# Performance work log

Hardware: AMD Instinct MI355X
Metric: run time of the kernel (lower is better)

Reference implementation:

```python
import jax, jax.numpy as jnp
import numpy as np

D_MAIN = 256
D_HID = 512  # int(d_main * d_multiplier)
N_NUM = 96
B = 1024
N_CAND = 100000
LN_EPS = 1e-5


def _ln(x, g, b):
    mu = x.mean(-1, keepdims=True)
    var = ((x - mu) ** 2).mean(-1, keepdims=True)
    return (x - mu) / jnp.sqrt(var + LN_EPS) * g + b


def _block(x, W1, b1, W2, b2):
    # Linear -> ReLU -> (Dropout=id) -> Linear -> (Dropout=id), residual added by caller
    return jnp.maximum(x @ W1 + b1, 0.0) @ W2 + b2


def setup_inputs() -> dict:
    key = jax.random.key(0)
    ks = jax.random.split(key, 32)

    def w(i, shape):
        fan_in = shape[0]
        return jax.random.normal(ks[i], shape, jnp.float32) / np.sqrt(fan_in)

    return {
        "x_num": jax.random.normal(ks[0], (B, N_NUM), jnp.float32),
        "cand_x_num": jax.random.normal(ks[1], (N_CAND, N_NUM), jnp.float32),
        "cand_y": jax.random.normal(ks[2], (N_CAND, 1), jnp.float32),
        "context_size": 96,
        # input linear
        "W_in": w(3, (N_NUM, D_MAIN)), "b_in": jnp.zeros((D_MAIN,), jnp.float32),
        # encoder block (no norm: first block)
        "We1": w(4, (D_MAIN, D_HID)), "be1": jnp.zeros((D_HID,), jnp.float32),
        "We2": w(5, (D_HID, D_MAIN)), "be2": jnp.zeros((D_MAIN,), jnp.float32),
        # mixer LayerNorm (mixer_normalization='auto' with encoder_n_blocks>0)
        "g_m": jnp.ones((D_MAIN,), jnp.float32), "b_m": jnp.zeros((D_MAIN,), jnp.float32),
        # S: key projection
        "Ws": w(6, (D_MAIN, D_MAIN)), "bs": jnp.zeros((D_MAIN,), jnp.float32),
        "Wy": w(7, (1, D_MAIN)), "by": jnp.zeros((D_MAIN,), jnp.float32),
        # V_t: Linear(no bias) -> ReLU -> Linear
        "Wt1": w(8, (D_MAIN, D_HID)),
        "Wt2": w(9, (D_HID, D_MAIN)), "bt2": jnp.zeros((D_MAIN,), jnp.float32),
        # predictor block (no norm: first block)
        "Wp1": w(10, (D_MAIN, D_HID)), "bp1": jnp.zeros((D_HID,), jnp.float32),
        "Wp2": w(11, (D_HID, D_MAIN)), "bp2": jnp.zeros((D_MAIN,), jnp.float32),
        # head P: LayerNorm -> ReLU -> Linear(d_main, 1)
        "g_h": jnp.ones((D_MAIN,), jnp.float32), "b_h": jnp.zeros((D_MAIN,), jnp.float32),
        "Wh": w(12, (D_MAIN, 1)), "bh": jnp.zeros((1,), jnp.float32),
    }


def _encode(x, W_in, b_in, We1, be1, We2, be2, g_m, b_m, Ws, bs):
    h = x @ W_in + b_in
    h = h + _block(h, We1, be1, We2, be2)
    k = _ln(h, g_m, b_m) @ Ws + bs
    return h, k


def reference(x_num, cand_x_num, cand_y, context_size,
              W_in, b_in, We1, be1, We2, be2, g_m, b_m, Ws, bs,
              Wy, by, Wt1, Wt2, bt2, Wp1, bp1, Wp2, bp2, g_h, b_h, Wh, bh):
    # encode queries and candidates with shared weights
    x, k = _encode(x_num, W_in, b_in, We1, be1, We2, be2, g_m, b_m, Ws, bs)
    _, ck = _encode(cand_x_num, W_in, b_in, We1, be1, We2, be2, g_m, b_m, Ws, bs)

    # similarities = -||k - ck||^2  [B, N_CAND]
    sim = (2.0 * (k @ ck.T)
           - (k * k).sum(-1, keepdims=True)
           - (ck * ck).sum(-1)[None, :])

    top_sim, idx = jax.lax.top_k(sim, context_size)   # [B, m]
    probs = jax.nn.softmax(top_sim, axis=-1)           # context_dropout = id in eval

    ctx_k = ck[idx]                                    # [B, m, d_main]
    ctx_y = cand_y[idx]                                # [B, m, 1]

    # values = V_y(y) + V_t(k - ctx_k)
    v = (ctx_y @ Wy + by
         + jnp.maximum((k[:, None, :] - ctx_k) @ Wt1, 0.0) @ Wt2 + bt2)

    x = x + jnp.einsum('bm,bmd->bd', probs, v)

    # predictor block + head
    x = x + _block(x, Wp1, bp1, Wp2, bp2)
    out = jnp.maximum(_ln(x, g_h, b_h), 0.0) @ Wh + bh  # [B, 1]
    return out
```

## Files before the change

### kernel.cpp

```cpp
#include <hip/hip_runtime.h>
#include <stdint.h>

#define NCAND 100000
#define NB    1024
#define DNUM  96
#define DM    256
#define DH    512
#define MCTX  96
#define LNEPS 1e-5f

typedef __bf16 bf16x8 __attribute__((ext_vector_type(8)));
typedef float  f32x4  __attribute__((ext_vector_type(4)));
typedef unsigned short u16x8 __attribute__((ext_vector_type(8)));
typedef unsigned short us;

__device__ __forceinline__ us f2bf(float x)
{
    unsigned u = __float_as_uint(x);
    unsigned r = u + 0x7FFFu + ((u >> 16) & 1u);
    return (us)(r >> 16);
}
__device__ __forceinline__ float bfbits(us h)
{
    return __uint_as_float(((unsigned)h) << 16);
}

extern "C" __global__ __launch_bounds__(256)
void split_k(const float* X, us* Xh, us* Xl, long long n)
{
    long long i = (long long)blockIdx.x * 256 + threadIdx.x;
    if (i < n) {
        float x = X[i];
        us h = f2bf(x);
        Xh[i] = h;
        Xl[i] = f2bf(x - bfbits(h));
    }
}

extern "C" __global__ __launch_bounds__(256)
void packW_k(const float* W, us* Ph, us* Pl, int Kd, int Nd)
{
    int i = blockIdx.x * 256 + threadIdx.x;
    if (i >= Kd * Nd) return;
    int e = i & 7, lane = (i >> 3) & 63, r = i >> 9;
    int KT = Kd >> 5;
    int kt = r % KT, jt = r / KT;
    int n = jt * 16 + (lane & 15);
    int k = kt * 32 + (lane >> 4) * 8 + e;
    float x = W[(long long)k * Nd + n];
    us h = f2bf(x);
    Ph[i] = h;
    Pl[i] = f2bf(x - bfbits(h));
}

extern "C" __global__ __launch_bounds__(256)
void packR_k(const us* Rh, const us* Rl, us* Ph, us* Pl, int Kd, int total)
{
    int i = blockIdx.x * 256 + threadIdx.x;
    if (i >= total) return;
    int e = i & 7, lane = (i >> 3) & 63, r = i >> 9;
    int KT = Kd >> 5;
    int kt = r % KT, jt = r / KT;
    int n = jt * 16 + (lane & 15);
    int k = kt * 32 + (lane >> 4) * 8 + e;
    Ph[i] = Rh[(long long)n * Kd + k];
    Pl[i] = Rl[(long long)n * Kd + k];
}

extern "C" __global__ __launch_bounds__(256)
void gemm_d(const us* Ah, const us* Al, const us* BPh, const us* BPl,
            float* outF, us* outH, us* outL, us* outB16,
            const float* bias, const us* Rh, const us* Rl, int dorelu,
            const float* lng, const float* lnb, us* lnH, us* lnL,
            float* snOut,
            const us* Gqh, const us* Gql, const us* Gch, const us* Gcl,
            const int* gidx,
            float* simT, const float* colb,
            int M, int N, int K)
{
    int t = threadIdx.x, wave = t >> 6, lane = t & 63;
    int lm = lane & 15, lk = (lane >> 4) * 8, rb = (lane >> 4) * 4;
    int m0 = blockIdx.x * 64 + wave * 16;
    int n0 = blockIdx.y * 256;
    int arow = m0 + lm;
    int KT = K >> 5;

    f32x4 acc[16];
#pragma unroll
    for (int j = 0; j < 16; j++)
        for (int e = 0; e < 4; e++) acc[j][e] = 0.0f;

    int gb = 0, gc = 0;
    if (gidx && arow < M) { gb = arow / MCTX; gc = gidx[arow]; }

    for (int kt = 0; kt < KT; kt++) {
        int k0 = kt * 32;
        u16x8 au = {0,0,0,0,0,0,0,0}, alu = au;
        if (arow < M) {
            if (!gidx) {
                au  = *(const u16x8*)(Ah + (long long)arow * K + k0 + lk);
                alu = *(const u16x8*)(Al + (long long)arow * K + k0 + lk);
            } else {
                u16x8 qh = *(const u16x8*)(Gqh + (long long)gb * DM + k0 + lk);
                u16x8 ql = *(const u16x8*)(Gql + (long long)gb * DM + k0 + lk);
                u16x8 ch = *(const u16x8*)(Gch + (long long)gc * DM + k0 + lk);
                u16x8 cl = *(const u16x8*)(Gcl + (long long)gc * DM + k0 + lk);
#pragma unroll
                for (int e = 0; e < 8; e++) {
                    float v = (bfbits(qh[e]) + bfbits(ql[e]))
                            - (bfbits(ch[e]) + bfbits(cl[e]));
                    au[e] = f2bf(v);
                }
            }
        }
        bf16x8 fah = *(bf16x8*)&au;
        bf16x8 fal = *(bf16x8*)&alu;
#pragma unroll
        for (int j = 0; j < 16; j++) {
            long long bo = ((long long)((n0 >> 4) + j) * KT + kt) * 512 + lane * 8;
            u16x8 bu  = *(const u16x8*)(BPh + bo);
            u16x8 blu = *(const u16x8*)(BPl + bo);
            bf16x8 fbh = *(bf16x8*)&bu;
            bf16x8 fbl = *(bf16x8*)&blu;
            acc[j] = __builtin_amdgcn_mfma_f32_16x16x32_bf16(fah, fbh, acc[j], 0, 0, 0);
            acc[j] = __builtin_amdgcn_mfma_f32_16x16x32_bf16(fah, fbl, acc[j], 0, 0, 0);
            if (!gidx)
                acc[j] = __builtin_amdgcn_mfma_f32_16x16x32_bf16(fal, fbh, acc[j], 0, 0, 0);
        }
    }

    if (simT) {
        if (m0 < M) {
#pragma unroll
            for (int j = 0; j < 16; j++) {
                int q = n0 + j * 16 + lm;
                f32x4 v;
                for (int e = 0; e < 4; e++)
                    v[e] = 2.0f * acc[j][e] - colb[m0 + rb + e];
                *(f32x4*)(simT + (long long)q * NCAND + m0 + rb) = v;
            }
        }
        return;
    }

#pragma unroll
    for (int j = 0; j < 16; j++) {
        int col = n0 + j * 16 + lm;
        float bc = bias ? bias[col] : 0.0f;
        for (int e = 0; e < 4; e++) {
            int row = m0 + rb + e;
            float v = acc[j][e] + bc;
            if (row < M) {
                long long oix = (long long)row * N + col;
                if (Rh) v += bfbits(Rh[oix]) + bfbits(Rl[oix]);
                if (dorelu && v < 0.0f) v = 0.0f;
                if (outF)   outF[oix] = v;
                if (outB16) outB16[oix] = f2bf(v);
                if (outH) { us h = f2bf(v); outH[oix] = h; outL[oix] = f2bf(v - bfbits(h)); }
            } else {
                if (dorelu && v < 0.0f) v = 0.0f;
            }
            acc[j][e] = v;
        }
    }

    if (lng || snOut) {
        float mu4[4], rs4[4];
        for (int e = 0; e < 4; e++) {
            float s1 = 0.0f, s2 = 0.0f;
#pragma unroll
            for (int j = 0; j < 16; j++) { float v = acc[j][e]; s1 += v; s2 += v * v; }
            for (int o = 1; o < 16; o <<= 1) {
                s1 += __shfl_xor(s1, o, 64);
                s2 += __shfl_xor(s2, o, 64);
            }
            int row = m0 + rb + e;
            if (snOut && lm == 0 && row < M) snOut[row] = s2;
            float mu = s1 * (1.0f / 256.0f);
            float var = s2 * (1.0f / 256.0f) - mu * mu;
            mu4[e] = mu;
            rs4[e] = rsqrtf(var + LNEPS);
        }
        if (lng) {
#pragma unroll
            for (int j = 0; j < 16; j++) {
                int col = n0 + j * 16 + lm;
                float g = lng[col], bb = lnb[col];
                for (int e = 0; e < 4; e++) {
                    int row = m0 + rb + e;
                    if (row >= M) continue;
                    float y = (acc[j][e] - mu4[e]) * rs4[e] * g + bb;
                    long long oix = (long long)row * N + col;
                    us h = f2bf(y);
                    lnH[oix] = h;
                    lnL[oix] = f2bf(y - bfbits(h));
                }
            }
        }
    }
}

__device__ unsigned fmapf(float f)
{
    unsigned u = __float_as_uint(f);
    return u ^ (unsigned)(((int)u >> 31) | (int)0x80000000);
}

extern "C" __global__ __launch_bounds__(1024)
void topk_k(const float* S, int q0, int* out_idx, float* out_p)
{
    int t = threadIdx.x;
    const float* row = S + (long long)blockIdx.x * NCAND;
    const float4* row4 = (const float4*)row;
    __shared__ int hist8[8][256];
    __shared__ unsigned sh_prefix;
    __shared__ int sh_want, cntG, cntE;
    __shared__ int   gidx[128];
    __shared__ float gval[128];
    __shared__ int   eqi[2048];
    __shared__ float vals[MCTX];
    __shared__ int   inds[MCTX];
    __shared__ float pr[MCTX];

    if (t == 0) { sh_prefix = 0u; sh_want = MCTX; cntG = 0; cntE = 0; }

    for (int lvl = 0; lvl < 4; lvl++) {
        int shift = 24 - 8 * lvl;
        for (int i = t; i < 2048; i += 1024) ((int*)hist8)[i] = 0;
        __syncthreads();
        unsigned prefix = sh_prefix;
        unsigned mask = (lvl == 0) ? 0u : (0xFFFFFFFFu << (shift + 8));
        int* hrow = hist8[t & 7];
        for (int c = t; c < NCAND / 4; c += 1024) {
            float4 v = row4[c];
            unsigned k0 = fmapf(v.x), k1 = fmapf(v.y), k2 = fmapf(v.z), k3 = fmapf(v.w);
            if ((k0 & mask) == prefix) atomicAdd(&hrow[(k0 >> shift) & 255], 1);
            if ((k1 & mask) == prefix) atomicAdd(&hrow[(k1 >> shift) & 255], 1);
            if ((k2 & mask) == prefix) atomicAdd(&hrow[(k2 >> shift) & 255], 1);
            if ((k3 & mask) == prefix) atomicAdd(&hrow[(k3 >> shift) & 255], 1);
        }
        __syncthreads();
        if (t < 256) {
            int s = 0;
            for (int g2 = 1; g2 < 8; g2++) s += hist8[g2][t];
            hist8[0][t] += s;
        }
        __syncthreads();
        if (t == 0) {
            int want = sh_want, cum = 0;
            for (int b2 = 255; b2 >= 0; b2--) {
                cum += hist8[0][b2];
                if (cum >= want) {
                    sh_want = want - (cum - hist8[0][b2]);
                    sh_prefix = prefix | ((unsigned)b2 << shift);
                    break;
                }
            }
        }
        __syncthreads();
    }
    unsigned T = sh_prefix;
    for (int c = t; c < NCAND / 4; c += 1024) {
        float4 v = row4[c];
        float vv[4]; vv[0] = v.x; vv[1] = v.y; vv[2] = v.z; vv[3] = v.w;
        for (int e = 0; e < 4; e++) {
            unsigned key = fmapf(vv[e]);
            if (key > T) {
                int p = atomicAdd(&cntG, 1);
                if (p < 128) { gidx[p] = c * 4 + e; gval[p] = vv[e]; }
            } else if (key == T) {
                int p = atomicAdd(&cntE, 1);
                if (p < 2048) eqi[p] = c * 4 + e;
            }
        }
    }
    __syncthreads();
    if (t == 0) {
        int nG = cntG; if (nG > MCTX) nG = MCTX;
        int nE = cntE; if (nE > 2048) nE = 2048;
        int need = MCTX - nG;
        for (int i = 0; i < nG; i++) { inds[i] = gidx[i]; vals[i] = gval[i]; }
        for (int s = 0; s < need; s++) {
            int best = 0x7FFFFFFF, bp = -1;
            for (int e = 0; e < nE; e++) if (eqi[e] < best) { best = eqi[e]; bp = e; }
            if (bp >= 0) { eqi[bp] = 0x7FFFFFFF; inds[nG + s] = best; vals[nG + s] = row[best]; }
            else         { inds[nG + s] = 0;     vals[nG + s] = -3.0e38f; }
        }
        float mx = -3.4e38f;
        for (int i = 0; i < MCTX; i++) if (vals[i] > mx) mx = vals[i];
        float sum = 0.0f;
        for (int i = 0; i < MCTX; i++) { float e = expf(vals[i] - mx); pr[i] = e; sum += e; }
        float inv = 1.0f / sum;
        for (int i = 0; i < MCTX; i++) pr[i] *= inv;
    }
    __syncthreads();
    if (t < MCTX) {
        long long o = (long long)(q0 + blockIdx.x) * MCTX + t;
        out_idx[o] = inds[t];
        out_p[o]   = pr[t];
    }
}

extern "C" __global__ __launch_bounds__(256)
void ybar_k(const float* P, const int* idx, const float* y, float* ybar)
{
    __shared__ float sred[256];
    int b = blockIdx.x, t = threadIdx.x;
    float v = 0.0f;
    if (t < MCTX) v = P[(long long)b * MCTX + t] * y[idx[(long long)b * MCTX + t]];
    sred[t] = v; __syncthreads();
    for (int s = 128; s > 0; s >>= 1) { if (t < s) sred[t] += sred[t + s]; __syncthreads(); }
    if (t == 0) ybar[b] = sred[0];
}

extern "C" __global__ __launch_bounds__(512)
void wsum2_k(const float* Pq, const float* R, const float* P, const int* idx, float* u)
{
    __shared__ float pl[MCTX];
    __shared__ int ix[MCTX];
    int b = blockIdx.x, j = threadIdx.x;
    if (j < MCTX) {
        pl[j] = P[(long long)b * MCTX + j];
        ix[j] = idx[(long long)b * MCTX + j];
    }
    __syncthreads();
    float pb = Pq[(long long)b * DH + j];
    float a = 0.0f;
    for (int m = 0; m < MCTX; m++) {
        float d = pb - R[(long long)ix[m] * DH + j];
        a += pl[m] * (d > 0.0f ? d : 0.0f);
    }
    u[(long long)b * DH + j] = a;
}

extern "C" __global__ __launch_bounds__(512)
void wsum_k(const us* U, const float* P, float* u)
{
    __shared__ float pl[MCTX];
    int b = blockIdx.x, j = threadIdx.x;
    if (j < MCTX) pl[j] = P[(long long)b * MCTX + j];
    __syncthreads();
    const us* Ub = U + (long long)b * MCTX * DH;
    float acc = 0.0f;
    for (int m = 0; m < MCTX; m++) acc += pl[m] * bfbits(Ub[(long long)m * DH + j]);
    u[(long long)b * DH + j] = acc;
}

extern "C" __global__ __launch_bounds__(256)
void mixprep_sp(us* h2h, us* h2l, const float* ybar,
                const float* Wy, const float* by, const float* bt2)
{
    int b = blockIdx.x, d = threadIdx.x;
    long long i = (long long)b * DM + d;
    float v = bfbits(h2h[i]) + bfbits(h2l[i]) + ybar[b] * Wy[d] + by[d] + bt2[d];
    us h = f2bf(v);
    h2h[i] = h;
    h2l[i] = f2bf(v - bfbits(h));
}

extern "C" __global__ __launch_bounds__(256)
void head_k(const float* X, const float* g, const float* bln, const float* Wh,
            const float* bh, float* out)
{
    __shared__ float sred[256];
    int r = blockIdx.x, t = threadIdx.x;
    float x = X[(long long)r * DM + t];
    sred[t] = x; __syncthreads();
    for (int s = 128; s > 0; s >>= 1) { if (t < s) sred[t] += sred[t + s]; __syncthreads(); }
    float mu = sred[0] * (1.0f / DM); __syncthreads();
    float d = x - mu;
    sred[t] = d * d; __syncthreads();
    for (int s = 128; s > 0; s >>= 1) { if (t < s) sred[t] += sred[t + s]; __syncthreads(); }
    float var = sred[0] * (1.0f / DM); __syncthreads();
    float ln = d * rsqrtf(var + LNEPS) * g[t] + bln[t];
    float rl = (ln > 0.0f) ? ln : 0.0f;
    sred[t] = rl * Wh[t]; __syncthreads();
    for (int s = 128; s > 0; s >>= 1) { if (t < s) sred[t] += sred[t + s]; __syncthreads(); }
    if (t == 0) out[r] = sred[0] + bh[0];
}

#define ZU (us*)0
#define ZCU (const us*)0
#define ZF (float*)0
#define ZCF (const float*)0
#define ZI (const int*)0

extern "C" void kernel_launch(void* const* d_in, const int* in_sizes, int n_in,
                              void* d_out, int out_size, void* d_ws, size_t ws_size,
                              hipStream_t stream)
{
    const float* x_num  = (const float*)d_in[0];
    const float* cand_x = (const float*)d_in[1];
    const float* cand_y = (const float*)d_in[2];
    const float* W_in = (const float*)d_in[4];
    const float* b_in = (const float*)d_in[5];
    const float* We1  = (const float*)d_in[6];
    const float* be1  = (const float*)d_in[7];
    const float* We2  = (const float*)d_in[8];
    const float* be2  = (const float*)d_in[9];
    const float* g_m  = (const float*)d_in[10];
    const float* b_m  = (const float*)d_in[11];
    const float* Ws   = (const float*)d_in[12];
    const float* bs   = (const float*)d_in[13];
    const float* Wy   = (const float*)d_in[14];
    const float* by   = (const float*)d_in[15];
    const float* Wt1  = (const float*)d_in[16];
    const float* Wt2  = (const float*)d_in[17];
    const float* bt2  = (const float*)d_in[18];
    const float* Wp1  = (const float*)d_in[19];
    const float* bp1  = (const float*)d_in[20];
    const float* Wp2  = (const float*)d_in[21];
    const float* bp2  = (const float*)d_in[22];
    const float* g_h  = (const float*)d_in[23];
    const float* b_h  = (const float*)d_in[24];
    const float* Wh   = (const float*)d_in[25];
    const float* bh   = (const float*)d_in[26];
    float* out = (float*)d_out;

    char* p = (char*)d_ws;
    us* WinPh = (us*)p; p += 256*96*2;   us* WinPl = (us*)p; p += 256*96*2;
    us* We1Ph = (us*)p; p += 512*256*2;  us* We1Pl = (us*)p; p += 512*256*2;
    us* We2Ph = (us*)p; p += 256*512*2;  us* We2Pl = (us*)p; p += 256*512*2;
    us* WsPh  = (us*)p; p += 256*256*2;  us* WsPl  = (us*)p; p += 256*256*2;
    us* Wt1Ph = (us*)p; p += 512*256*2;  us* Wt1Pl = (us*)p; p += 512*256*2;
    us* Wt2Ph = (us*)p; p += 256*512*2;  us* Wt2Pl = (us*)p; p += 256*512*2;
    us* Wp1Ph = (us*)p; p += 512*256*2;  us* Wp1Pl = (us*)p; p += 512*256*2;
    us* Wp2Ph = (us*)p; p += 256*512*2;  us* Wp2Pl = (us*)p; p += 256*512*2;
    us* XNh  = (us*)p; p += (long long)NB*DNUM*2;  us* XNl  = (us*)p; p += (long long)NB*DNUM*2;
    us* HQ1h = (us*)p; p += (long long)NB*DM*2;    us* HQ1l = (us*)p; p += (long long)NB*DM*2;
    us* TQh  = (us*)p; p += (long long)NB*DH*2;    us* TQl  = (us*)p; p += (long long)NB*DH*2;
    us* HQ2h = (us*)p; p += (long long)NB*DM*2;    us* HQ2l = (us*)p; p += (long long)NB*DM*2;
    us* LNQh = (us*)p; p += (long long)NB*DM*2;    us* LNQl = (us*)p; p += (long long)NB*DM*2;
    us* KQh  = (us*)p; p += (long long)NB*DM*2;    us* KQl  = (us*)p; p += (long long)NB*DM*2;
    us* KQPh = (us*)p; p += (long long)NB*DM*2;    us* KQPl = (us*)p; p += (long long)NB*DM*2;
    us* XQh  = (us*)p; p += (long long)NB*DM*2;    us* XQl  = (us*)p; p += (long long)NB*DM*2;
    us* UQvh = (us*)p; p += (long long)NB*DH*2;    us* UQvl = (us*)p; p += (long long)NB*DH*2;
    float* UQv  = (float*)p; p += (long long)NB*DH*4;
    float* Pq   = (float*)p; p += (long long)NB*DH*4;
    float* XQ2f = (float*)p; p += (long long)NB*DM*4;
    float* YB   = (float*)p; p += (long long)NB*4;
    int*   IDX  = (int*)p;   p += (long long)NB*MCTX*4;
    float* PRB  = (float*)p; p += (long long)NB*MCTX*4;
    us* KCh = (us*)p; p += (long long)NCAND*DM*2;  us* KCl = (us*)p; p += (long long)NCAND*DM*2;
    float* SC = (float*)p; p += (long long)NCAND*4;

    size_t used = (size_t)(p - (char*)d_ws);
    long long avail = (ws_size > used + 4096) ? (long long)(ws_size - used - 4096) : 0;
    int EC = 6250;
    if      (avail >= 243300000LL) EC = 50000;
    else if (avail >= 141000000LL) EC = 25000;
    else if (avail >=  89700000LL) EC = 12500;
    int QS = (avail >= 204800000LL) ? 512 : 256;
    int tierA = (avail >= 204800000LL) ? 1 : 0;
    int VC = (avail >= 100700000LL) ? 1024 : 512;

    char* AR = p;
    us* CXh = (us*)AR;
    us* CXl = CXh + (long long)NCAND*DNUM;
    char* EB = AR + (long long)NCAND*DNUM*4;
    us* Hch  = (us*)EB;                              us* Hcl  = Hch + (long long)EC*DM;
    us* Tch  = (us*)(EB + (long long)EC*DM*4);       us* Tcl  = Tch + (long long)EC*DH;
    us* LNch = (us*)(EB + (long long)EC*(DM+DH)*4);  us* LNcl = LNch + (long long)EC*DM;
    float* Sb = (float*)AR;
    float* R  = (float*)AR;
    us* Ub = (us*)AR;

    dim3 blk(256);

    packW_k<<<dim3((DNUM*DM+255)/256), blk, 0, stream>>>(W_in, WinPh, WinPl, DNUM, DM);
    packW_k<<<dim3((DM*DH+255)/256), blk, 0, stream>>>(We1, We1Ph, We1Pl, DM, DH);
    packW_k<<<dim3((DH*DM+255)/256), blk, 0, stream>>>(We2, We2Ph, We2Pl, DH, DM);
    packW_k<<<dim3((DM*DM+255)/256), blk, 0, stream>>>(Ws,  WsPh,  WsPl,  DM, DM);
    packW_k<<<dim3((DM*DH+255)/256), blk, 0, stream>>>(Wt1, Wt1Ph, Wt1Pl, DM, DH);
    packW_k<<<dim3((DH*DM+255)/256), blk, 0, stream>>>(Wt2, Wt2Ph, Wt2Pl, DH, DM);
    packW_k<<<dim3((DM*DH+255)/256), blk, 0, stream>>>(Wp1, Wp1Ph, Wp1Pl, DM, DH);
    packW_k<<<dim3((DH*DM+255)/256), blk, 0, stream>>>(Wp2, Wp2Ph, Wp2Pl, DH, DM);
    split_k<<<dim3((NB*DNUM+255)/256), blk, 0, stream>>>(x_num, XNh, XNl, (long long)NB*DNUM);
    split_k<<<dim3((NCAND*DNUM+255)/256), blk, 0, stream>>>(cand_x, CXh, CXl, (long long)NCAND*DNUM);

    gemm_d<<<dim3(NB/64, 1), blk, 0, stream>>>(XNh, XNl, WinPh, WinPl,
        ZF, HQ1h, HQ1l, ZU, b_in, ZCU, ZCU, 0, ZCF, ZCF, ZU, ZU, ZF,
        ZCU, ZCU, ZCU, ZCU, ZI, ZF, ZCF, NB, DM, DNUM);
    gemm_d<<<dim3(NB/64, 2), blk, 0, stream>>>(HQ1h, HQ1l, We1Ph, We1Pl,
        ZF, TQh, TQl, ZU, be1, ZCU, ZCU, 1, ZCF, ZCF, ZU, ZU, ZF,
        ZCU, ZCU, ZCU, ZCU, ZI, ZF, ZCF, NB, DH, DM);
    gemm_d<<<dim3(NB/64, 1), blk, 0, stream>>>(TQh, TQl, We2Ph, We2Pl,
        ZF, HQ2h, HQ2l, ZU, be2, HQ1h, HQ1l, 0, g_m, b_m, LNQh, LNQl, ZF,
        ZCU, ZCU, ZCU, ZCU, ZI, ZF, ZCF, NB, DM, DH);
    gemm_d<<<dim3(NB/64, 1), blk, 0, stream>>>(LNQh, LNQl, WsPh, WsPl,
        ZF, KQh, KQl, ZU, bs, ZCU, ZCU, 0, ZCF, ZCF, ZU, ZU, ZF,
        ZCU, ZCU, ZCU, ZCU, ZI, ZF, ZCF, NB, DM, DM);
    packR_k<<<dim3((NB*DM+255)/256), blk, 0, stream>>>(KQh, KQl, KQPh, KQPl, DM, NB*DM);

    for (int c0 = 0; c0 < NCAND; c0 += EC) {
        int gx = (EC + 63) / 64;
        gemm_d<<<dim3(gx, 1), blk, 0, stream>>>(CXh + (long long)c0*DNUM, CXl + (long long)c0*DNUM,
            WinPh, WinPl, ZF, Hch, Hcl, ZU, b_in, ZCU, ZCU, 0, ZCF, ZCF, ZU, ZU, ZF,
            ZCU, ZCU, ZCU, ZCU, ZI, ZF, ZCF, EC, DM, DNUM);
        gemm_d<<<dim3(gx, 2), blk, 0, stream>>>(Hch, Hcl, We1Ph, We1Pl,
            ZF, Tch, Tcl, ZU, be1, ZCU, ZCU, 1, ZCF, ZCF, ZU, ZU, ZF,
            ZCU, ZCU, ZCU, ZCU, ZI, ZF, ZCF, EC, DH, DM);
        gemm_d<<<dim3(gx, 1), blk, 0, stream>>>(Tch, Tcl, We2Ph, We2Pl,
            ZF, ZU, ZU, ZU, be2, Hch, Hcl, 0, g_m, b_m, LNch, LNcl, ZF,
            ZCU, ZCU, ZCU, ZCU, ZI, ZF, ZCF, EC, DM, DH);
        gemm_d<<<dim3(gx, 1), blk, 0, stream>>>(LNch, LNcl, WsPh, WsPl,
            ZF, KCh + (long long)c0*DM, KCl + (long long)c0*DM, ZU, bs, ZCU, ZCU, 0,
            ZCF, ZCF, ZU, ZU, SC + c0,
            ZCU, ZCU, ZCU, ZCU, ZI, ZF, ZCF, EC, DM, DM);
    }

    for (int q0 = 0; q0 < NB; q0 += QS) {
        gemm_d<<<dim3((NCAND + 63) / 64, QS / 256), blk, 0, stream>>>(KCh, KCl,
            KQPh + (long long)q0*DM, KQPl + (long long)q0*DM,
            ZF, ZU, ZU, ZU, ZCF, ZCU, ZCU, 0, ZCF, ZCF, ZU, ZU, ZF,
            ZCU, ZCU, ZCU, ZCU, ZI, Sb, SC, NCAND, QS, DM);
        topk_k<<<dim3(QS), dim3(1024), 0, stream>>>(Sb, q0, IDX, PRB);
    }

    ybar_k<<<dim3(NB), blk, 0, stream>>>(PRB, IDX, cand_y, YB);
    gemm_d<<<dim3(NB/64, 2), blk, 0, stream>>>(KQh, KQl, Wt1Ph, Wt1Pl,
        Pq, ZU, ZU, ZU, ZCF, ZCU, ZCU, 0, ZCF, ZCF, ZU, ZU, ZF,
        ZCU, ZCU, ZCU, ZCU, ZI, ZF, ZCF, NB, DH, DM);
    if (tierA) {
        gemm_d<<<dim3((NCAND + 63) / 64, 2), blk, 0, stream>>>(KCh, KCl, Wt1Ph, Wt1Pl,
            R, ZU, ZU, ZU, ZCF, ZCU, ZCU, 0, ZCF, ZCF, ZU, ZU, ZF,
            ZCU, ZCU, ZCU, ZCU, ZI, ZF, ZCF, NCAND, DH, DM);
        wsum2_k<<<dim3(NB), dim3(512), 0, stream>>>(Pq, R, PRB, IDX, UQv);
    } else {
        for (int v0 = 0; v0 < NB; v0 += VC) {
            gemm_d<<<dim3((VC * MCTX) / 64, 2), blk, 0, stream>>>(ZCU, ZCU, Wt1Ph, Wt1Pl,
                ZF, ZU, ZU, Ub, ZCF, ZCU, ZCU, 1, ZCF, ZCF, ZU, ZU, ZF,
                KQh + (long long)v0*DM, KQl + (long long)v0*DM, KCh, KCl,
                IDX + (long long)v0*MCTX, ZF, ZCF, VC * MCTX, DH, DM);
            wsum_k<<<dim3(VC), dim3(512), 0, stream>>>(Ub, PRB + (long long)v0*MCTX,
                                                       UQv + (long long)v0*DH);
        }
    }
    split_k<<<dim3((NB*DH+255)/256), blk, 0, stream>>>(UQv, UQvh, UQvl, (long long)NB*DH);
    mixprep_sp<<<dim3(NB), blk, 0, stream>>>(HQ2h, HQ2l, YB, Wy, by, bt2);
    gemm_d<<<dim3(NB/64, 1), blk, 0, stream>>>(UQvh, UQvl, Wt2Ph, Wt2Pl,
        ZF, XQh, XQl, ZU, ZCF, HQ2h, HQ2l, 0, ZCF, ZCF, ZU, ZU, ZF,
        ZCU, ZCU, ZCU, ZCU, ZI, ZF, ZCF, NB, DM, DH);

    gemm_d<<<dim3(NB/64, 2), blk, 0, stream>>>(XQh, XQl, Wp1Ph, Wp1Pl,
        ZF, TQh, TQl, ZU, bp1, ZCU, ZCU, 1, ZCF, ZCF, ZU, ZU, ZF,
        ZCU, ZCU, ZCU, ZCU, ZI, ZF, ZCF, NB, DH, DM);
    gemm_d<<<dim3(NB/64, 1), blk, 0, stream>>>(TQh, TQl, Wp2Ph, Wp2Pl,
        XQ2f, ZU, ZU, ZU, bp2, XQh, XQl, 0, ZCF, ZCF, ZU, ZU, ZF,
        ZCU, ZCU, ZCU, ZCU, ZI, ZF, ZCF, NB, DM, DH);
    head_k<<<dim3(NB), blk, 0, stream>>>(XQ2f, g_h, b_h, Wh, bh, out);
}
```

Before: 3.561 ms.

## Use 12-bit radix pass with compacted candidate refinement in top-k; stage A tiles in LDS

The top-k kernel replaces four full passes of 8-bit radix histograms over the 100k similarity row with one 12-bit histogram pass. Elements in the boundary bin are compacted into shared memory, and the remaining radix levels run only on that small set, with a fallback to full-row passes when the set overflows. The aim is to cut repeated global reads and atomics per row. Separately, the GEMM now loads the A tile cooperatively into LDS and reads fragments from there, which adds two barriers per k-step.

```diff
diff --git a/kernel.cpp b/kernel.cpp
--- a/kernel.cpp
+++ b/kernel.cpp
@@ -8,6 +8,7 @@
 #define DH    512
 #define MCTX  96
 #define LNEPS 1e-5f
+#define ECAP  2560
 
 typedef __bf16 bf16x8 __attribute__((ext_vector_type(8)));
 typedef float  f32x4  __attribute__((ext_vector_type(4)));
@@ -78,11 +79,13 @@
             float* simT, const float* colb,
             int M, int N, int K)
 {
+    __shared__ us Ahs[64][40];
+    __shared__ us Als[64][40];
     int t = threadIdx.x, wave = t >> 6, lane = t & 63;
     int lm = lane & 15, lk = (lane >> 4) * 8, rb = (lane >> 4) * 4;
-    int m0 = blockIdx.x * 64 + wave * 16;
+    int m0b = blockIdx.x * 64;
+    int m0 = m0b + wave * 16;
     int n0 = blockIdx.y * 256;
-    int arow = m0 + lm;
     int KT = K >> 5;
 
     f32x4 acc[16];
@@ -90,31 +93,38 @@
     for (int j = 0; j < 16; j++)
         for (int e = 0; e < 4; e++) acc[j][e] = 0.0f;
 
+    int sr = t >> 2;
+    int ss = (t & 3) * 8;
+    int srow = m0b + sr;
     int gb = 0, gc = 0;
-    if (gidx && arow < M) { gb = arow / MCTX; gc = gidx[arow]; }
+    if (gidx && srow < M) { gb = srow / MCTX; gc = gidx[srow]; }
 
     for (int kt = 0; kt < KT; kt++) {
         int k0 = kt * 32;
-        u16x8 au = {0,0,0,0,0,0,0,0}, alu = au;
-        if (arow < M) {
+        u16x8 ah8 = {0,0,0,0,0,0,0,0}, al8 = ah8;
+        if (srow < M) {
             if (!gidx) {
-                au  = *(const u16x8*)(Ah + (long long)arow * K + k0 + lk);
-                alu = *(const u16x8*)(Al + (long long)arow * K + k0 + lk);
+                ah8 = *(const u16x8*)(Ah + (long long)srow * K + k0 + ss);
+                al8 = *(const u16x8*)(Al + (long long)srow * K + k0 + ss);
             } else {
-                u16x8 qh = *(const u16x8*)(Gqh + (long long)gb * DM + k0 + lk);
-                u16x8 ql = *(const u16x8*)(Gql + (long long)gb * DM + k0 + lk);
-                u16x8 ch = *(const u16x8*)(Gch + (long long)gc * DM + k0 + lk);
-                u16x8 cl = *(const u16x8*)(Gcl + (long long)gc * DM + k0 + lk);
+                u16x8 qh = *(const u16x8*)(Gqh + (long long)gb * DM + k0 + ss);
+                u16x8 ql = *(const u16x8*)(Gql + (long long)gb * DM + k0 + ss);
+                u16x8 ch = *(const u16x8*)(Gch + (long long)gc * DM + k0 + ss);
+                u16x8 cl = *(const u16x8*)(Gcl + (long long)gc * DM + k0 + ss);
 #pragma unroll
                 for (int e = 0; e < 8; e++) {
                     float v = (bfbits(qh[e]) + bfbits(ql[e]))
                             - (bfbits(ch[e]) + bfbits(cl[e]));
-                    au[e] = f2bf(v);
+                    ah8[e] = f2bf(v);
                 }
             }
         }
-        bf16x8 fah = *(bf16x8*)&au;
-        bf16x8 fal = *(bf16x8*)&alu;
+        __syncthreads();
+        *(u16x8*)&Ahs[sr][ss] = ah8;
+        *(u16x8*)&Als[sr][ss] = al8;
+        __syncthreads();
+        bf16x8 fah = *(const bf16x8*)&Ahs[wave * 16 + lm][lk];
+        bf16x8 fal = *(const bf16x8*)&Als[wave * 16 + lm][lk];
 #pragma unroll
         for (int j = 0; j < 16; j++) {
             long long bo = ((long long)((n0 >> 4) + j) * KT + kt) * 512 + lane * 8;
@@ -205,6 +215,11 @@
     unsigned u = __float_as_uint(f);
     return u ^ (unsigned)(((int)u >> 31) | (int)0x80000000);
 }
+__device__ float funmap(unsigned key)
+{
+    unsigned uu = (key & 0x80000000u) ? (key ^ 0x80000000u) : ~key;
+    return __uint_as_float(uu);
+}
 
 extern "C" __global__ __launch_bounds__(1024)
 void topk_k(const float* S, int q0, int* out_idx, float* out_p)
@@ -212,91 +227,165 @@
     int t = threadIdx.x;
     const float* row = S + (long long)blockIdx.x * NCAND;
     const float4* row4 = (const float4*)row;
-    __shared__ int hist8[8][256];
-    __shared__ unsigned sh_prefix;
-    __shared__ int sh_want, cntG, cntE;
-    __shared__ int   gidx[128];
-    __shared__ float gval[128];
-    __shared__ int   eqi[2048];
-    __shared__ float vals[MCTX];
-    __shared__ int   inds[MCTX];
+    __shared__ int hist[4096];
+    __shared__ unsigned ek0[ECAP]; __shared__ int ei0[ECAP];
+    __shared__ unsigned ek1[ECAP]; __shared__ int ei1[ECAP];
+    __shared__ float gv[MCTX]; __shared__ int gi[MCTX];
     __shared__ float pr[MCTX];
-
-    if (t == 0) { sh_prefix = 0u; sh_want = MCTX; cntG = 0; cntE = 0; }
-
-    for (int lvl = 0; lvl < 4; lvl++) {
-        int shift = 24 - 8 * lvl;
-        for (int i = t; i < 2048; i += 1024) ((int*)hist8)[i] = 0;
-        __syncthreads();
-        unsigned prefix = sh_prefix;
-        unsigned mask = (lvl == 0) ? 0u : (0xFFFFFFFFu << (shift + 8));
-        int* hrow = hist8[t & 7];
-        for (int c = t; c < NCAND / 4; c += 1024) {
-            float4 v = row4[c];
-            unsigned k0 = fmapf(v.x), k1 = fmapf(v.y), k2 = fmapf(v.z), k3 = fmapf(v.w);
-            if ((k0 & mask) == prefix) atomicAdd(&hrow[(k0 >> shift) & 255], 1);
-            if ((k1 & mask) == prefix) atomicAdd(&hrow[(k1 >> shift) & 255], 1);
-            if ((k2 & mask) == prefix) atomicAdd(&hrow[(k2 >> shift) & 255], 1);
-            if ((k3 & mask) == prefix) atomicAdd(&hrow[(k3 >> shift) & 255], 1);
-        }
-        __syncthreads();
-        if (t < 256) {
-            int s = 0;
-            for (int g2 = 1; g2 < 8; g2++) s += hist8[g2][t];
-            hist8[0][t] += s;
-        }
-        __syncthreads();
-        if (t == 0) {
-            int want = sh_want, cum = 0;
-            for (int b2 = 255; b2 >= 0; b2--) {
-                cum += hist8[0][b2];
-                if (cum >= want) {
-                    sh_want = want - (cum - hist8[0][b2]);
-                    sh_prefix = prefix | ((unsigned)b2 << shift);
-                    break;
-                }
-            }
-        }
-        __syncthreads();
-    }
-    unsigned T = sh_prefix;
+    __shared__ int gcnt, ecnt, encnt, sh_b, sh_need;
+
+    if (t == 0) { gcnt = 0; ecnt = 0; }
+    for (int i = t; i < 4096; i += 1024) hist[i] = 0;
+    __syncthreads();
+
+    for (int c = t; c < NCAND / 4; c += 1024) {
+        float4 v = row4[c];
+        atomicAdd(&hist[fmapf(v.x) >> 20], 1);
+        atomicAdd(&hist[fmapf(v.y) >> 20], 1);
+        atomicAdd(&hist[fmapf(v.z) >> 20], 1);
+        atomicAdd(&hist[fmapf(v.w) >> 20], 1);
+    }
+    __syncthreads();
+    if (t == 0) {
+        int cum = 0, b = 4095;
+        for (; b >= 0; b--) { cum += hist[b]; if (cum >= MCTX) break; }
+        sh_b = b; sh_need = MCTX - (cum - hist[b]);
+    }
+    __syncthreads();
+    unsigned b1 = (unsigned)sh_b;
     for (int c = t; c < NCAND / 4; c += 1024) {
         float4 v = row4[c];
         float vv[4]; vv[0] = v.x; vv[1] = v.y; vv[2] = v.z; vv[3] = v.w;
         for (int e = 0; e < 4; e++) {
             unsigned key = fmapf(vv[e]);
-            if (key > T) {
-                int p = atomicAdd(&cntG, 1);
-                if (p < 128) { gidx[p] = c * 4 + e; gval[p] = vv[e]; }
-            } else if (key == T) {
-                int p = atomicAdd(&cntE, 1);
-                if (p < 2048) eqi[p] = c * 4 + e;
+            unsigned bin = key >> 20;
+            if (bin > b1) {
+                int p = atomicAdd(&gcnt, 1);
+                gv[p] = vv[e]; gi[p] = c * 4 + e;
+            } else if (bin == b1) {
+                int p = atomicAdd(&ecnt, 1);
+                if (p < ECAP) { ek0[p] = key; ei0[p] = c * 4 + e; }
             }
         }
     }
     __syncthreads();
+    unsigned pref = b1 << 20;
+    int shifts[3]; shifts[0] = 12; shifts[1] = 4; shifts[2] = 0;
+    int widths[3]; widths[0] = 256; widths[1] = 256; widths[2] = 16;
+
+    if (ecnt <= ECAP) {
+        int n = ecnt;
+        unsigned* ksrc = ek0; int* isrc = ei0;
+        unsigned* kdst = ek1; int* idst = ei1;
+        for (int lvl = 0; lvl < 3; lvl++) {
+            int sh = shifts[lvl], nb = widths[lvl];
+            unsigned msk = (unsigned)(nb - 1);
+            for (int i = t; i < nb; i += 1024) hist[i] = 0;
+            if (t == 0) encnt = 0;
+            __syncthreads();
+            for (int i = t; i < n; i += 1024)
+                atomicAdd(&hist[(ksrc[i] >> sh) & msk], 1);
+            __syncthreads();
+            if (t == 0) {
+                int need = sh_need, cum = 0, b = nb - 1;
+                for (; b >= 0; b--) { cum += hist[b]; if (cum >= need) break; }
+                sh_b = b; sh_need = need - (cum - hist[b]);
+            }
+            __syncthreads();
+            unsigned bl = (unsigned)sh_b;
+            for (int i = t; i < n; i += 1024) {
+                unsigned bin = (ksrc[i] >> sh) & msk;
+                if (bin > bl) {
+                    int p = atomicAdd(&gcnt, 1);
+                    gv[p] = funmap(ksrc[i]); gi[p] = isrc[i];
+                } else if (bin == bl) {
+                    int p = atomicAdd(&encnt, 1);
+                    kdst[p] = ksrc[i]; idst[p] = isrc[i];
+                }
+            }
+            __syncthreads();
+            pref |= bl << sh;
+            n = encnt;
+            unsigned* tk = ksrc; ksrc = kdst; kdst = tk;
+            int* ti = isrc; isrc = idst; idst = ti;
+            __syncthreads();
+        }
+        if (t == 0) {
+            int need = sh_need;
+            float tv = funmap(pref);
+            for (int s = 0; s < need; s++) {
+                int best = 0x7FFFFFFF, bp = -1;
+                for (int i2 = 0; i2 < n; i2++) if (isrc[i2] < best) { best = isrc[i2]; bp = i2; }
+                int p = gcnt + s;
+                if (bp >= 0) { isrc[bp] = 0x7FFFFFFF; gv[p] = tv; gi[p] = best; }
+                else         { gv[p] = -3.0e38f; gi[p] = 0; }
+            }
+        }
+        __syncthreads();
+    } else {
+        unsigned mask = 0xFFF00000u;
+        for (int lvl = 0; lvl < 3; lvl++) {
+            int sh = shifts[lvl], nb = widths[lvl];
+            unsigned msk = (unsigned)(nb - 1);
+            for (int i = t; i < nb; i += 1024) hist[i] = 0;
+            __syncthreads();
+            for (int c = t; c < NCAND; c += 1024) {
+                unsigned key = fmapf(row[c]);
+                if ((key & mask) == pref) atomicAdd(&hist[(key >> sh) & msk], 1);
+            }
+            __syncthreads();
+            if (t == 0) {
+                int need = sh_need, cum = 0, b = nb - 1;
+                for (; b >= 0; b--) { cum += hist[b]; if (cum >= need) break; }
+                sh_b = b; sh_need = need - (cum - hist[b]);
+            }
+            __syncthreads();
+            pref |= ((unsigned)sh_b) << sh;
+            mask |= msk << sh;
+            __syncthreads();
+        }
+        if (t == 0) encnt = 0;
+        __syncthreads();
+        for (int c = t; c < NCAND; c += 1024) {
+            unsigned key = fmapf(row[c]);
+            if ((key >> 20) == b1) {
+                if (key > pref) {
+                    int p = atomicAdd(&gcnt, 1);
+                    gv[p] = row[c]; gi[p] = c;
+                } else if (key == pref) {
+                    int p = atomicAdd(&encnt, 1);
+                    if (p < ECAP) ei1[p] = c;
+                }
+            }
+        }
+        __syncthreads();
+        if (t == 0) {
+            int need = sh_need;
+            int n = encnt; if (n > ECAP) n = ECAP;
+            float tv = funmap(pref);
+            for (int s = 0; s < need; s++) {
+                int best = 0x7FFFFFFF, bp = -1;
+                for (int i2 = 0; i2 < n; i2++) if (ei1[i2] < best) { best = ei1[i2]; bp = i2; }
+                int p = gcnt + s;
+                if (bp >= 0) { ei1[bp] = 0x7FFFFFFF; gv[p] = tv; gi[p] = best; }
+                else         { gv[p] = -3.0e38f; gi[p] = 0; }
+            }
+        }
+        __syncthreads();
+    }
+
     if (t == 0) {
-        int nG = cntG; if (nG > MCTX) nG = MCTX;
-        int nE = cntE; if (nE > 2048) nE = 2048;
-        int need = MCTX - nG;
-        for (int i = 0; i < nG; i++) { inds[i] = gidx[i]; vals[i] = gval[i]; }
-        for (int s = 0; s < need; s++) {
-            int best = 0x7FFFFFFF, bp = -1;
-            for (int e = 0; e < nE; e++) if (eqi[e] < best) { best = eqi[e]; bp = e; }
-            if (bp >= 0) { eqi[bp] = 0x7FFFFFFF; inds[nG + s] = best; vals[nG + s] = row[best]; }
-            else         { inds[nG + s] = 0;     vals[nG + s] = -3.0e38f; }
-        }
         float mx = -3.4e38f;
-        for (int i = 0; i < MCTX; i++) if (vals[i] > mx) mx = vals[i];
+        for (int i = 0; i < MCTX; i++) if (gv[i] > mx) mx = gv[i];
         float sum = 0.0f;
-        for (int i = 0; i < MCTX; i++) { float e = expf(vals[i] - mx); pr[i] = e; sum += e; }
+        for (int i = 0; i < MCTX; i++) { float e = expf(gv[i] - mx); pr[i] = e; sum += e; }
         float inv = 1.0f / sum;
         for (int i = 0; i < MCTX; i++) pr[i] *= inv;
     }
     __syncthreads();
     if (t < MCTX) {
         long long o = (long long)(q0 + blockIdx.x) * MCTX + t;
-        out_idx[o] = inds[t];
+        out_idx[o] = gi[t];
         out_p[o]   = pr[t];
     }
 }
```

Measured after the change: 3.946 ms. 1.11x slower.

## Retile GEMM waves to 64x64 subtiles for A/B fragment reuse

Applied to the files above, without the earlier changes.

Each wave now computes a 64-row by 64-column subtile (4x4 MFMA tiles) instead of 16 rows by 256 columns, so every loaded A fragment is reused across 4 B tiles and every B fragment across 4 A rows. This cuts per-wave B-fragment global loads from 16 to 4 per k-step, at the cost of 4 A-fragment loads (including the gathered difference computation). Row LayerNorm statistics now span waves, so a shared-memory cross-wave reduction with two barriers is added. The simT epilogue indexing changes accordingly.

```diff
diff --git a/kernel.cpp b/kernel.cpp
--- a/kernel.cpp
+++ b/kernel.cpp
@@ -78,122 +78,164 @@
             float* simT, const float* colb,
             int M, int N, int K)
 {
+    __shared__ float red1[256];
+    __shared__ float red2[256];
+    __shared__ float mu_s[64];
+    __shared__ float rs_s[64];
     int t = threadIdx.x, wave = t >> 6, lane = t & 63;
     int lm = lane & 15, lk = (lane >> 4) * 8, rb = (lane >> 4) * 4;
-    int m0 = blockIdx.x * 64 + wave * 16;
+    int m0b = blockIdx.x * 64;
     int n0 = blockIdx.y * 256;
-    int arow = m0 + lm;
     int KT = K >> 5;
-
-    f32x4 acc[16];
-#pragma unroll
-    for (int j = 0; j < 16; j++)
-        for (int e = 0; e < 4; e++) acc[j][e] = 0.0f;
-
-    int gb = 0, gc = 0;
-    if (gidx && arow < M) { gb = arow / MCTX; gc = gidx[arow]; }
+    int jt0 = (n0 >> 4) + wave * 4;
+
+    f32x4 acc[4][4];
+#pragma unroll
+    for (int i = 0; i < 4; i++)
+#pragma unroll
+        for (int j = 0; j < 4; j++)
+            for (int e = 0; e < 4; e++) acc[i][j][e] = 0.0f;
+
+    int gb4[4], gc4[4];
+    if (gidx) {
+#pragma unroll
+        for (int i = 0; i < 4; i++) {
+            int grow = m0b + i * 16 + lm;
+            if (grow < M) { gb4[i] = grow / MCTX; gc4[i] = gidx[grow]; }
+            else          { gb4[i] = 0; gc4[i] = 0; }
+        }
+    }
 
     for (int kt = 0; kt < KT; kt++) {
         int k0 = kt * 32;
-        u16x8 au = {0,0,0,0,0,0,0,0}, alu = au;
-        if (arow < M) {
-            if (!gidx) {
-                au  = *(const u16x8*)(Ah + (long long)arow * K + k0 + lk);
-                alu = *(const u16x8*)(Al + (long long)arow * K + k0 + lk);
-            } else {
-                u16x8 qh = *(const u16x8*)(Gqh + (long long)gb * DM + k0 + lk);
-                u16x8 ql = *(const u16x8*)(Gql + (long long)gb * DM + k0 + lk);
-                u16x8 ch = *(const u16x8*)(Gch + (long long)gc * DM + k0 + lk);
-                u16x8 cl = *(const u16x8*)(Gcl + (long long)gc * DM + k0 + lk);
-#pragma unroll
-                for (int e = 0; e < 8; e++) {
-                    float v = (bfbits(qh[e]) + bfbits(ql[e]))
-                            - (bfbits(ch[e]) + bfbits(cl[e]));
-                    au[e] = f2bf(v);
+        bf16x8 fah[4], fal[4];
+#pragma unroll
+        for (int i = 0; i < 4; i++) {
+            int arow = m0b + i * 16 + lm;
+            u16x8 ah8 = {0,0,0,0,0,0,0,0}, al8 = ah8;
+            if (arow < M) {
+                if (!gidx) {
+                    ah8 = *(const u16x8*)(Ah + (long long)arow * K + k0 + lk);
+                    al8 = *(const u16x8*)(Al + (long long)arow * K + k0 + lk);
+                } else {
+                    u16x8 qh = *(const u16x8*)(Gqh + (long long)gb4[i] * DM + k0 + lk);
+                    u16x8 ql = *(const u16x8*)(Gql + (long long)gb4[i] * DM + k0 + lk);
+                    u16x8 ch = *(const u16x8*)(Gch + (long long)gc4[i] * DM + k0 + lk);
+                    u16x8 cl = *(const u16x8*)(Gcl + (long long)gc4[i] * DM + k0 + lk);
+#pragma unroll
+                    for (int e = 0; e < 8; e++) {
+                        float v = (bfbits(qh[e]) + bfbits(ql[e]))
+                                - (bfbits(ch[e]) + bfbits(cl[e]));
+                        ah8[e] = f2bf(v);
+                    }
                 }
             }
-        }
-        bf16x8 fah = *(bf16x8*)&au;
-        bf16x8 fal = *(bf16x8*)&alu;
-#pragma unroll
-        for (int j = 0; j < 16; j++) {
-            long long bo = ((long long)((n0 >> 4) + j) * KT + kt) * 512 + lane * 8;
+            fah[i] = *(bf16x8*)&ah8;
+            fal[i] = *(bf16x8*)&al8;
+        }
+#pragma unroll
+        for (int j = 0; j < 4; j++) {
+            long long bo = ((long long)(jt0 + j) * KT + kt) * 512 + lane * 8;
             u16x8 bu  = *(const u16x8*)(BPh + bo);
             u16x8 blu = *(const u16x8*)(BPl + bo);
             bf16x8 fbh = *(bf16x8*)&bu;
             bf16x8 fbl = *(bf16x8*)&blu;
-            acc[j] = __builtin_amdgcn_mfma_f32_16x16x32_bf16(fah, fbh, acc[j], 0, 0, 0);
-            acc[j] = __builtin_amdgcn_mfma_f32_16x16x32_bf16(fah, fbl, acc[j], 0, 0, 0);
-            if (!gidx)
-                acc[j] = __builtin_amdgcn_mfma_f32_16x16x32_bf16(fal, fbh, acc[j], 0, 0, 0);
+#pragma unroll
+            for (int i = 0; i < 4; i++) {
+                acc[i][j] = __builtin_amdgcn_mfma_f32_16x16x32_bf16(fah[i], fbh, acc[i][j], 0, 0, 0);
+                acc[i][j] = __builtin_amdgcn_mfma_f32_16x16x32_bf16(fah[i], fbl, acc[i][j], 0, 0, 0);
+                if (!gidx)
+                    acc[i][j] = __builtin_amdgcn_mfma_f32_16x16x32_bf16(fal[i], fbh, acc[i][j], 0, 0, 0);
+            }
         }
     }
 
     if (simT) {
-        if (m0 < M) {
-#pragma unroll
-            for (int j = 0; j < 16; j++) {
-                int q = n0 + j * 16 + lm;
+#pragma unroll
+        for (int i = 0; i < 4; i++) {
+            int cb = m0b + i * 16;
+            if (cb >= M) break;
+#pragma unroll
+            for (int j = 0; j < 4; j++) {
+                int q = n0 + wave * 64 + j * 16 + lm;
                 f32x4 v;
                 for (int e = 0; e < 4; e++)
-                    v[e] = 2.0f * acc[j][e] - colb[m0 + rb + e];
-                *(f32x4*)(simT + (long long)q * NCAND + m0 + rb) = v;
+                    v[e] = 2.0f * acc[i][j][e] - colb[cb + rb + e];
+                *(f32x4*)(simT + (long long)q * NCAND + cb + rb) = v;
             }
         }
         return;
     }
 
 #pragma unroll
-    for (int j = 0; j < 16; j++) {
-        int col = n0 + j * 16 + lm;
+    for (int j = 0; j < 4; j++) {
+        int col = n0 + wave * 64 + j * 16 + lm;
         float bc = bias ? bias[col] : 0.0f;
-        for (int e = 0; e < 4; e++) {
-            int row = m0 + rb + e;
-            float v = acc[j][e] + bc;
-            if (row < M) {
-                long long oix = (long long)row * N + col;
-                if (Rh) v += bfbits(Rh[oix]) + bfbits(Rl[oix]);
-                if (dorelu && v < 0.0f) v = 0.0f;
-                if (outF)   outF[oix] = v;
-                if (outB16) outB16[oix] = f2bf(v);
-                if (outH) { us h = f2bf(v); outH[oix] = h; outL[oix] = f2bf(v - bfbits(h)); }
-            } else {
-                if (dorelu && v < 0.0f) v = 0.0f;
-            }
-            acc[j][e] = v;
+#pragma unroll
+        for (int i = 0; i < 4; i++) {
+            for (int e = 0; e < 4; e++) {
+                int row = m0b + i * 16 + rb + e;
+                float v = acc[i][j][e] + bc;
+                if (row < M) {
+                    long long oix = (long long)row * N + col;
+                    if (Rh) v += bfbits(Rh[oix]) + bfbits(Rl[oix]);
+                    if (dorelu && v < 0.0f) v = 0.0f;
+                    if (outF)   outF[oix] = v;
+                    if (outB16) outB16[oix] = f2bf(v);
+                    if (outH) { us h = f2bf(v); outH[oix] = h; outL[oix] = f2bf(v - bfbits(h)); }
+                } else {
+                    if (dorelu && v < 0.0f) v = 0.0f;
+                }
+                acc[i][j][e] = v;
+            }
         }
     }
 
     if (lng || snOut) {
-        float mu4[4], rs4[4];
-        for (int e = 0; e < 4; e++) {
-            float s1 = 0.0f, s2 = 0.0f;
-#pragma unroll
-            for (int j = 0; j < 16; j++) { float v = acc[j][e]; s1 += v; s2 += v * v; }
-            for (int o = 1; o < 16; o <<= 1) {
-                s1 += __shfl_xor(s1, o, 64);
-                s2 += __shfl_xor(s2, o, 64);
-            }
-            int row = m0 + rb + e;
-            if (snOut && lm == 0 && row < M) snOut[row] = s2;
-            float mu = s1 * (1.0f / 256.0f);
-            float var = s2 * (1.0f / 256.0f) - mu * mu;
-            mu4[e] = mu;
-            rs4[e] = rsqrtf(var + LNEPS);
-        }
+#pragma unroll
+        for (int i = 0; i < 4; i++) {
+            for (int e = 0; e < 4; e++) {
+                int lr = i * 16 + rb + e;
+                float s1 = 0.0f, s2 = 0.0f;
+#pragma unroll
+                for (int j = 0; j < 4; j++) { float v = acc[i][j][e]; s1 += v; s2 += v * v; }
+                for (int o = 1; o < 16; o <<= 1) {
+                    s1 += __shfl_xor(s1, o, 64);
+                    s2 += __shfl_xor(s2, o, 64);
+                }
+                if (lm == 0) { red1[lr * 4 + wave] = s1; red2[lr * 4 + wave] = s2; }
+            }
+        }
+        __syncthreads();
+        if (t < 64) {
+            float a = red1[t*4] + red1[t*4+1] + red1[t*4+2] + red1[t*4+3];
+            float b2 = red2[t*4] + red2[t*4+1] + red2[t*4+2] + red2[t*4+3];
+            if (lng) {
+                float mu = a * (1.0f / 256.0f);
+                float var = b2 * (1.0f / 256.0f) - mu * mu;
+                mu_s[t] = mu;
+                rs_s[t] = rsqrtf(var + LNEPS);
+            }
+            if (snOut && (m0b + t) < M) snOut[m0b + t] = b2;
+        }
+        __syncthreads();
         if (lng) {
 #pragma unroll
-            for (int j = 0; j < 16; j++) {
-                int col = n0 + j * 16 + lm;
+            for (int j = 0; j < 4; j++) {
+                int col = n0 + wave * 64 + j * 16 + lm;
                 float g = lng[col], bb = lnb[col];
-                for (int e = 0; e < 4; e++) {
-                    int row = m0 + rb + e;
-                    if (row >= M) continue;
-                    float y = (acc[j][e] - mu4[e]) * rs4[e] * g + bb;
-                    long long oix = (long long)row * N + col;
-                    us h = f2bf(y);
-                    lnH[oix] = h;
-                    lnL[oix] = f2bf(y - bfbits(h));
+#pragma unroll
+                for (int i = 0; i < 4; i++) {
+                    for (int e = 0; e < 4; e++) {
+                        int lr = i * 16 + rb + e;
+                        int row = m0b + lr;
+                        if (row >= M) continue;
+                        float y = (acc[i][j][e] - mu_s[lr]) * rs_s[lr] * g + bb;
+                        long long oix = (long long)row * N + col;
+                        us h = f2bf(y);
+                        lnH[oix] = h;
+                        lnL[oix] = f2bf(y - bfbits(h));
+                    }
                 }
             }
         }
```

Result: faster. 3.463 ms (-2.8%).
